# Kernel tuning notes

Measured on AMD Instinct MI355X. Metric: run time of the kernel, lower is better.

## Reference

```python
import jax, jax.numpy as jnp
import numpy as np

B, N, T, D = 4, 256, 64, 128
DR, DH = 32, 128  # d_relation, d_hidden


def setup_inputs() -> dict:
    key = jax.random.key(0)
    ks = jax.random.split(key, 12)
    s = 0.05
    return {
        "H": jax.random.normal(ks[0], (B, N, T, D), jnp.float32),
        "R": jax.random.normal(ks[1], (B, N, N, DR), jnp.float32),
        "delta_H": jax.random.normal(ks[2], (B, N, T, D), jnp.float32),
        # params (torch Linear convention: W @ x + b with W shape (out, in))
        "Wq": jax.random.normal(ks[3], (DH, D), jnp.float32) * s,
        "bq": jnp.zeros((DH,), jnp.float32),
        "Wk": jax.random.normal(ks[4], (DH, D), jnp.float32) * s,
        "bk": jnp.zeros((DH,), jnp.float32),
        "Wr": jax.random.normal(ks[5], (DH, DR), jnp.float32) * s,
        "br": jnp.zeros((DH,), jnp.float32),
        "Wf": jax.random.normal(ks[6], (D, 3 * D + DR), jnp.float32) * s,
        "bf": jnp.zeros((D,), jnp.float32),
        "gamma": jnp.ones((D,), jnp.float32),
        "beta": jnp.zeros((D,), jnp.float32),
    }


def reference(H, R, delta_H, Wq, bq, Wk, bk, Wr, br, Wf, bf, gamma, beta):
    Bm, Nn, Tt, Dd = H.shape
    dr = R.shape[-1]

    # projections (eval mode: dropout is identity)
    q = jnp.einsum('bitd,hd->bith', H, Wq) + bq           # (B,N,T,DH)
    k = jnp.einsum('bjtd,hd->bjth', H, Wk) + bk           # (B,N,T,DH)
    rproj = jnp.einsum('bijr,hr->bijh', R, Wr) + br       # (B,N,N,DH)

    # attn_score[b,i,j,t] = <q_i[t], k_j[t] + Wr(r_ij)> / sqrt(d_model)
    scores = (jnp.einsum('bith,bjth->bijt', q, k)
              + jnp.einsum('bith,bijh->bijt', q, rproj)) / jnp.sqrt(jnp.asarray(Dd, H.dtype))
    w = jax.nn.softmax(scores, axis=-1)                   # softmax over time t
    # exclude the j == i pair (original loop skips it)
    w = w * (1.0 - jnp.eye(Nn, dtype=w.dtype))[None, :, :, None]

    # fuse Linear decomposed over the concat [h_i, h_j, r_ij, sum_t delta_h_j]
    W1 = Wf[:, :Dd]                 # acts on h_i
    W2 = Wf[:, Dd:2 * Dd]           # acts on h_j
    W3 = Wf[:, 2 * Dd:2 * Dd + dr]  # acts on r_ij
    W4 = Wf[:, 2 * Dd + dr:]        # acts on delta sum

    A = jnp.einsum('bitd,ed->bite', H, W1)                       # (B,N,T,D)
    Bj = jnp.einsum('bjtd,ed->bjte', H, W2)                      # (B,N,T,D)
    Cij = jnp.einsum('bijr,er->bije', R, W3)                     # (B,N,N,D)
    Ej = jnp.einsum('bjd,ed->bje', delta_H.sum(axis=2), W4)      # (B,N,D)

    wsum = w.sum(axis=2)                                         # (B,N,T)
    z = ((A + bf) * wsum[..., None]
         + jnp.einsum('bijt,bjte->bite', w, Bj)
         + jnp.einsum('bijt,bije->bite', w, Cij)
         + jnp.einsum('bijt,bje->bite', w, Ej))

    # residual + LayerNorm over last dim
    x = H + z
    mu = x.mean(axis=-1, keepdims=True)
    var = x.var(axis=-1, keepdims=True)
    return (x - mu) / jnp.sqrt(var + 1e-5) * gamma + beta
```

## Files before the change

kernel.cpp:

```cpp
#include <hip/hip_runtime.h>

typedef __attribute__((ext_vector_type(4))) float f32x4;
typedef __attribute__((ext_vector_type(8))) short short8;

constexpr int NB = 4, NS = 256, NT = 64, ND = 128, NR = 32;
constexpr int WFR = 3 * ND + NR;
constexpr float SCALE = 0.08838834764831845f;

__device__ __forceinline__ unsigned short f2bf(float f) {
  unsigned x = __float_as_uint(f);
  return (unsigned short)((x + 0x7FFFu + ((x >> 16) & 1u)) >> 16);
}
__device__ __forceinline__ float bf2f(unsigned short u) {
  return __uint_as_float((unsigned)u << 16);
}

__global__ __launch_bounds__(256) void kP(const float* __restrict__ Wq,
    const float* __restrict__ Wk, const float* __restrict__ Wr,
    const float* __restrict__ br, const float* __restrict__ bq,
    const float* __restrict__ Wf,
    unsigned short* __restrict__ Wqb, unsigned short* __restrict__ Wkb,
    unsigned short* __restrict__ W1b, unsigned short* __restrict__ W2b,
    unsigned short* __restrict__ W3b, unsigned short* __restrict__ Wqrt,
    float* __restrict__ Gbias) {
  const int blk = blockIdx.x, tid = threadIdx.x;
  if (blk < 64) {
    const int which = blk >> 4;
    const int idx = ((blk & 15) * 256 + tid) * 4;
    const int e = idx >> 7, d = idx & 127;
    float4 v;
    unsigned short* dst;
    if (which == 0)      { v = *(const float4*)&Wq[idx];            dst = Wqb; }
    else if (which == 1) { v = *(const float4*)&Wk[idx];            dst = Wkb; }
    else if (which == 2) { v = *(const float4*)&Wf[e * WFR + d];        dst = W1b; }
    else                 { v = *(const float4*)&Wf[e * WFR + ND + d];   dst = W2b; }
    dst[idx + 0] = f2bf(v.x); dst[idx + 1] = f2bf(v.y);
    dst[idx + 2] = f2bf(v.z); dst[idx + 3] = f2bf(v.w);
  } else if (blk < 68) {
    const int idx = ((blk - 64) * 256 + tid) * 4;
    const int e = idx >> 5, r = idx & 31;
    float4 v = *(const float4*)&Wf[e * WFR + 2 * ND + r];
    W3b[idx + 0] = f2bf(v.x); W3b[idx + 1] = f2bf(v.y);
    W3b[idx + 2] = f2bf(v.z); W3b[idx + 3] = f2bf(v.w);
  } else {
    const int rr = blk - 68;
    __shared__ float Vl[128];
    __shared__ float gbl[128];
    if (tid < 128) {
      float v = 0.f;
      if (rr < 32) v = Wr[tid * 32 + rr];
      else if (rr == 32) v = br[tid];
      Vl[tid] = v;
      gbl[tid] = bq[tid] * v;
    }
    __syncthreads();
    if (tid < 128) {
      float acc = 0.f;
      #pragma unroll 8
      for (int h = 0; h < 128; ++h) acc += Wq[h * 128 + tid] * Vl[h];
      Wqrt[rr * 128 + tid] = f2bf(acc * SCALE);
    }
    if (tid == 0) {
      float g = 0.f;
      for (int h = 0; h < 128; ++h) g += gbl[h];
      Gbias[rr] = g * SCALE;
    }
  }
}

__global__ __launch_bounds__(128) void kA(const float* __restrict__ dH,
                                          const float* __restrict__ Wf,
                                          float* __restrict__ Ej) {
  __shared__ float ds[ND];
  const int bj = blockIdx.x;
  const int d = threadIdx.x;
  const float* p = dH + (size_t)bj * NT * ND + d;
  float s = 0.f;
  #pragma unroll 8
  for (int t = 0; t < NT; ++t) s += p[t * ND];
  ds[d] = s;
  __syncthreads();
  const float* w4 = Wf + (size_t)d * WFR + 2 * ND + NR;
  float acc = 0.f;
  #pragma unroll 8
  for (int dd = 0; dd < ND; ++dd) acc += ds[dd] * w4[dd];
  Ej[(size_t)bj * ND + d] = acc;
}

__global__ __launch_bounds__(256) void kR(const float* __restrict__ R,
                                          unsigned short* __restrict__ Rb,
                                          unsigned short* __restrict__ Rtb) {
  __shared__ unsigned short rt[256 * 34];
  const int bi = blockIdx.x, tid = threadIdx.x;
  const float* src = R + (size_t)bi * 8192;
  #pragma unroll
  for (int it = 0; it < 8; ++it) {
    const int idx = (tid + it * 256) * 4;
    const float4 v = *(const float4*)&src[idx];
    const unsigned short s0 = f2bf(v.x), s1 = f2bf(v.y);
    const unsigned short s2 = f2bf(v.z), s3 = f2bf(v.w);
    unsigned long long p = (unsigned long long)s0 | ((unsigned long long)s1 << 16)
                         | ((unsigned long long)s2 << 32) | ((unsigned long long)s3 << 48);
    *(unsigned long long*)&Rb[(size_t)bi * 8192 + idx] = p;
    const int j = idx >> 5, r = idx & 31;
    *(unsigned*)&rt[j * 34 + r]     = (unsigned)s0 | ((unsigned)s1 << 16);
    *(unsigned*)&rt[j * 34 + r + 2] = (unsigned)s2 | ((unsigned)s3 << 16);
  }
  __syncthreads();
  #pragma unroll
  for (int it = 0; it < 4; ++it) {
    const int flat = (tid + it * 256) * 8;
    const int r = flat >> 8, j0 = flat & 255;
    short8 o;
    #pragma unroll
    for (int u = 0; u < 8; ++u) o[u] = (short)rt[(j0 + u) * 34 + r];
    *(short8*)&Rtb[(size_t)bi * 8192 + flat] = o;
  }
}

__device__ __forceinline__ void gemm_tile(const short8 (&afr)[4][4],
    const unsigned short* __restrict__ Wp, int nt, int l15, int l4,
    f32x4 (&acc)[4]) {
  #pragma unroll
  for (int mt = 0; mt < 4; ++mt) acc[mt] = (f32x4){0.f, 0.f, 0.f, 0.f};
  #pragma unroll
  for (int kt = 0; kt < 4; ++kt) {
    short8 bfr = *(const short8*)(Wp + (16 * nt + l15) * 128 + 32 * kt + 8 * l4);
    #pragma unroll
    for (int mt = 0; mt < 4; ++mt)
      acc[mt] = __builtin_amdgcn_mfma_f32_16x16x32_bf16(afr[mt][kt], bfr, acc[mt], 0, 0, 0);
  }
}

__device__ __forceinline__ void gemm_tile2(const short8 (&afr)[2][4],
    const unsigned short* __restrict__ Wp, int nt, int l15, int l4,
    f32x4 (&acc)[2]) {
  #pragma unroll
  for (int mt = 0; mt < 2; ++mt) acc[mt] = (f32x4){0.f, 0.f, 0.f, 0.f};
  #pragma unroll
  for (int kt = 0; kt < 4; ++kt) {
    short8 bfr = *(const short8*)(Wp + (16 * nt + l15) * 128 + 32 * kt + 8 * l4);
    #pragma unroll
    for (int mt = 0; mt < 2; ++mt)
      acc[mt] = __builtin_amdgcn_mfma_f32_16x16x32_bf16(afr[mt][kt], bfr, acc[mt], 0, 0, 0);
  }
}

__global__ __launch_bounds__(256) void kB(const float* __restrict__ H,
    const unsigned short* __restrict__ W1b, const unsigned short* __restrict__ W2b,
    const unsigned short* __restrict__ Wqrt, const float* __restrict__ Gbias,
    const float* __restrict__ bf, const float* __restrict__ Ej,
    unsigned short* __restrict__ Apbb, unsigned short* __restrict__ BEb,
    unsigned short* __restrict__ Gb) {
  __shared__ unsigned short st[2][64 * 136];
  const int bn = blockIdx.x, tid = threadIdx.x;
  const int b = bn >> 8, n = bn & 255;
  const int lane = tid & 63, wv = tid >> 6;
  const int l15 = lane & 15, l4 = lane >> 4;
  short8 afr[4][4];
  const float* hb = H + (size_t)bn * (NT * ND);
  #pragma unroll
  for (int mt = 0; mt < 4; ++mt)
    #pragma unroll
    for (int kt = 0; kt < 4; ++kt) {
      const float* p = hb + (16 * mt + l15) * ND + 32 * kt + 8 * l4;
      float4 u0 = *(const float4*)p;
      float4 u1 = *(const float4*)(p + 4);
      short8 f;
      f[0] = (short)f2bf(u0.x); f[1] = (short)f2bf(u0.y);
      f[2] = (short)f2bf(u0.z); f[3] = (short)f2bf(u0.w);
      f[4] = (short)f2bf(u1.x); f[5] = (short)f2bf(u1.y);
      f[6] = (short)f2bf(u1.z); f[7] = (short)f2bf(u1.w);
      afr[mt][kt] = f;
    }
  f32x4 acc[4];
  #pragma unroll 1
  for (int pass = 0; pass < 2; ++pass) {
    const unsigned short* W = (pass == 0) ? W1b : W2b;
    unsigned short* buf = st[pass];
    #pragma unroll
    for (int n2 = 0; n2 < 2; ++n2) {
      const int nt = 2 * wv + n2, c = 16 * nt + l15;
      gemm_tile(afr, W, nt, l15, l4, acc);
      const float bias = (pass == 0) ? bf[c] : Ej[(size_t)bn * 128 + c];
      #pragma unroll
      for (int mt = 0; mt < 4; ++mt)
        #pragma unroll
        for (int jr = 0; jr < 4; ++jr)
          buf[(16 * mt + 4 * l4 + jr) * 136 + c] = f2bf(acc[mt][jr] + bias);
    }
  }
  if (wv < 3) {
    const int nt = wv, c = 16 * nt + l15;
    gemm_tile(afr, Wqrt, nt, l15, l4, acc);
    const float bias = Gbias[c];
    #pragma unroll
    for (int mt = 0; mt < 4; ++mt)
      #pragma unroll
      for (int jr = 0; jr < 4; ++jr) {
        const int tr = 16 * mt + 4 * l4 + jr;
        Gb[(size_t)bn * 3072 + tr * 48 + c] = f2bf(acc[mt][jr] + bias);
      }
  }
  __syncthreads();
  #pragma unroll
  for (int it = 0; it < 4; ++it) {
    const int flat = tid * 8 + it * 2048;
    const int row = flat >> 7, col = flat & 127;
    *(short8*)&Apbb[(size_t)bn * 8192 + flat] = *(const short8*)&st[0][row * 136 + col];
    *(short8*)&BEb[((size_t)(b * 64 + row) * 256 + n) * 128 + col] =
        *(const short8*)&st[1][row * 136 + col];
  }
}

__global__ __launch_bounds__(512) void kQK(const float* __restrict__ H,
    const unsigned short* __restrict__ Wqb, const unsigned short* __restrict__ Wkb,
    const float* __restrict__ bq, const float* __restrict__ bk,
    unsigned short* __restrict__ Sb) {
  __shared__ unsigned short qs[256 * 136];
  __shared__ unsigned short ks[256 * 136];
  const int bt = blockIdx.x;
  const int b = bt >> 6, t = bt & 63;
  const int tid = threadIdx.x, lane = tid & 63, wv = tid >> 6;
  const int l15 = lane & 15, l4 = lane >> 4;
  short8 afr[2][4];
  #pragma unroll
  for (int mt = 0; mt < 2; ++mt)
    #pragma unroll
    for (int kt = 0; kt < 4; ++kt) {
      const int n = 32 * wv + 16 * mt + l15;
      const float* p = &H[(((size_t)(b * 256 + n)) * 64 + t) * 128 + 32 * kt + 8 * l4];
      float4 u0 = *(const float4*)p;
      float4 u1 = *(const float4*)(p + 4);
      short8 f;
      f[0] = (short)f2bf(u0.x); f[1] = (short)f2bf(u0.y);
      f[2] = (short)f2bf(u0.z); f[3] = (short)f2bf(u0.w);
      f[4] = (short)f2bf(u1.x); f[5] = (short)f2bf(u1.y);
      f[6] = (short)f2bf(u1.z); f[7] = (short)f2bf(u1.w);
      afr[mt][kt] = f;
    }
  f32x4 acc[2];
  #pragma unroll 1
  for (int pass = 0; pass < 2; ++pass) {
    const unsigned short* W = (pass == 0) ? Wqb : Wkb;
    const float* bp = (pass == 0) ? bq : bk;
    unsigned short* dst = (pass == 0) ? qs : ks;
    #pragma unroll
    for (int nt = 0; nt < 8; ++nt) {
      gemm_tile2(afr, W, nt, l15, l4, acc);
      const int c = 16 * nt + l15;
      const float bias = bp[c];
      #pragma unroll
      for (int mt = 0; mt < 2; ++mt)
        #pragma unroll
        for (int jr = 0; jr < 4; ++jr)
          dst[(32 * wv + 16 * mt + 4 * l4 + jr) * 136 + c] = f2bf(acc[mt][jr] + bias);
    }
  }
  __syncthreads();
  short8 qa[2][4];
  #pragma unroll
  for (int mt = 0; mt < 2; ++mt)
    #pragma unroll
    for (int kt = 0; kt < 4; ++kt)
      qa[mt][kt] = *(const short8*)&qs[(32 * wv + 16 * mt + l15) * 136 + 32 * kt + 8 * l4];
  unsigned short* buf = qs + wv * (32 * 136);
  #pragma unroll 1
  for (int jh = 0; jh < 2; ++jh) {
    f32x4 sacc[2][8];
    #pragma unroll
    for (int mi = 0; mi < 2; ++mi)
      #pragma unroll
      for (int ntj = 0; ntj < 8; ++ntj) sacc[mi][ntj] = (f32x4){0.f, 0.f, 0.f, 0.f};
    #pragma unroll
    for (int kt = 0; kt < 4; ++kt) {
      short8 bb[8];
      #pragma unroll
      for (int ntj = 0; ntj < 8; ++ntj)
        bb[ntj] = *(const short8*)&ks[(16 * (8 * jh + ntj) + l15) * 136 + 32 * kt + 8 * l4];
      #pragma unroll
      for (int mi = 0; mi < 2; ++mi)
        #pragma unroll
        for (int ntj = 0; ntj < 8; ++ntj)
          sacc[mi][ntj] = __builtin_amdgcn_mfma_f32_16x16x32_bf16(qa[mi][kt], bb[ntj], sacc[mi][ntj], 0, 0, 0);
    }
    #pragma unroll
    for (int mi = 0; mi < 2; ++mi)
      #pragma unroll
      for (int ntj = 0; ntj < 8; ++ntj)
        #pragma unroll
        for (int jr = 0; jr < 4; ++jr)
          buf[(16 * mi + 4 * l4 + jr) * 136 + 16 * ntj + l15] =
              f2bf(sacc[mi][ntj][jr] * SCALE);
    #pragma unroll
    for (int it = 0; it < 8; ++it) {
      const int flat = lane * 8 + it * 512;
      const int row = flat >> 7, col = flat & 127;
      *(short8*)&Sb[((size_t)bt * 256 + 32 * wv + row) * 256 + 128 * jh + col] =
          *(const short8*)&buf[row * 136 + col];
    }
  }
}

__global__ __launch_bounds__(256) void kSM(
    const unsigned short* __restrict__ Gb, const unsigned short* __restrict__ Rb,
    const unsigned short* __restrict__ Rtb, const unsigned short* __restrict__ Sb,
    const unsigned short* __restrict__ W3b, unsigned short* __restrict__ Apbb,
    unsigned short* __restrict__ Wbw) {
  __shared__ unsigned short wl[64 * 264];
  __shared__ unsigned short Ml[4][16 * 40];
  __shared__ float wred[4][64];
  __shared__ float wsl[64];
  const int bi = blockIdx.x, b = bi >> 8, i = bi & 255;
  const int tid = threadIdx.x, lane = tid & 63, wv = tid >> 6;
  const int l15 = lane & 15, l4 = lane >> 4;
  const f32x4 zz = (f32x4){0.f, 0.f, 0.f, 0.f};

  #pragma unroll
  for (int it = 0; it < 8; ++it) {
    const int flat = tid * 8 + it * 2048;
    const int t = flat >> 8, col = flat & 255;
    *(short8*)&wl[t * 264 + col] =
        *(const short8*)&Sb[(((size_t)b * 64 + t) * 256 + i) * 256 + col];
  }

  short8 ga[4];
  #pragma unroll
  for (int mt = 0; mt < 4; ++mt)
    ga[mt] = *(const short8*)(Gb + ((size_t)bi * 64 + 16 * mt + l15) * 48 + 8 * l4);
  f32x4 acc[4][4];
  #pragma unroll
  for (int nt = 0; nt < 4; ++nt) {
    const int j = 64 * wv + 16 * nt + l15;
    short8 rb = *(const short8*)(Rb + ((size_t)bi * 256 + j) * 32 + 8 * l4);
    #pragma unroll
    for (int mt = 0; mt < 4; ++mt)
      acc[mt][nt] = __builtin_amdgcn_mfma_f32_16x16x32_bf16(ga[mt], rb, zz, 0, 0, 0);
  }
  float qbr[4][4];
  #pragma unroll
  for (int mt = 0; mt < 4; ++mt)
    #pragma unroll
    for (int jr = 0; jr < 4; ++jr)
      qbr[mt][jr] = bf2f(Gb[((size_t)bi * 64 + 16 * mt + 4 * l4 + jr) * 48 + 32]);

  __syncthreads();

  #pragma unroll
  for (int mt = 0; mt < 4; ++mt)
    #pragma unroll
    for (int nt = 0; nt < 4; ++nt)
      #pragma unroll
      for (int jr = 0; jr < 4; ++jr)
        acc[mt][nt][jr] += bf2f(wl[(16 * mt + 4 * l4 + jr) * 264 + 64 * wv + 16 * nt + l15])
                         + qbr[mt][jr];

  #pragma unroll
  for (int nt = 0; nt < 4; ++nt) {
    float mx = -1e30f;
    #pragma unroll
    for (int mt = 0; mt < 4; ++mt)
      #pragma unroll
      for (int jr = 0; jr < 4; ++jr) mx = fmaxf(mx, acc[mt][nt][jr]);
    mx = fmaxf(mx, __shfl_xor(mx, 16));
    mx = fmaxf(mx, __shfl_xor(mx, 32));
    float sm = 0.f;
    #pragma unroll
    for (int mt = 0; mt < 4; ++mt)
      #pragma unroll
      for (int jr = 0; jr < 4; ++jr) {
        const float e = __expf(acc[mt][nt][jr] - mx);
        acc[mt][nt][jr] = e;
        sm += e;
      }
    sm += __shfl_xor(sm, 16);
    sm += __shfl_xor(sm, 32);
    const int j = 64 * wv + 16 * nt + l15;
    const float inv = (j == i) ? 0.f : 1.f / sm;
    #pragma unroll
    for (int mt = 0; mt < 4; ++mt)
      #pragma unroll
      for (int jr = 0; jr < 4; ++jr) acc[mt][nt][jr] *= inv;
  }

  float part[4][4];
  #pragma unroll
  for (int mt = 0; mt < 4; ++mt)
    #pragma unroll
    for (int jr = 0; jr < 4; ++jr) {
      float s = 0.f;
      #pragma unroll
      for (int nt = 0; nt < 4; ++nt) s += acc[mt][nt][jr];
      part[mt][jr] = s;
    }
  #pragma unroll
  for (int m = 1; m < 16; m <<= 1)
    #pragma unroll
    for (int mt = 0; mt < 4; ++mt)
      #pragma unroll
      for (int jr = 0; jr < 4; ++jr) part[mt][jr] += __shfl_xor(part[mt][jr], m);
  if (l15 == 0) {
    #pragma unroll
    for (int mt = 0; mt < 4; ++mt)
      #pragma unroll
      for (int jr = 0; jr < 4; ++jr) wred[wv][16 * mt + 4 * l4 + jr] = part[mt][jr];
  }

  #pragma unroll
  for (int mt = 0; mt < 4; ++mt)
    #pragma unroll
    for (int nt = 0; nt < 4; ++nt)
      #pragma unroll
      for (int jr = 0; jr < 4; ++jr)
        wl[(16 * mt + 4 * l4 + jr) * 264 + 64 * wv + 16 * nt + l15] =
            f2bf(acc[mt][nt][jr]);

  __syncthreads();

  if (tid < 64) wsl[tid] = wred[0][tid] + wred[1][tid] + wred[2][tid] + wred[3][tid];

  #pragma unroll
  for (int it = 0; it < 8; ++it) {
    const int flat = tid * 8 + it * 2048;
    const int t = flat >> 8, j = flat & 255;
    *(short8*)&Wbw[(((size_t)(b * 64 + t)) * 256 + i) * 256 + j] =
        *(const short8*)&wl[t * 264 + j];
  }

  f32x4 mac[2];
  mac[0] = zz; mac[1] = zz;
  #pragma unroll
  for (int kt = 0; kt < 8; ++kt) {
    short8 a = *(const short8*)&wl[(16 * wv + l15) * 264 + 32 * kt + 8 * l4];
    #pragma unroll
    for (int nt = 0; nt < 2; ++nt) {
      short8 bb = *(const short8*)(Rtb + ((size_t)bi * 32 + 16 * nt + l15) * 256 + 32 * kt + 8 * l4);
      mac[nt] = __builtin_amdgcn_mfma_f32_16x16x32_bf16(a, bb, mac[nt], 0, 0, 0);
    }
  }
  #pragma unroll
  for (int nt = 0; nt < 2; ++nt)
    #pragma unroll
    for (int jr = 0; jr < 4; ++jr)
      Ml[wv][(4 * l4 + jr) * 40 + 16 * nt + l15] = f2bf(mac[nt][jr]);
  asm volatile("s_waitcnt lgkmcnt(0)" ::: "memory");
  short8 a2 = *(const short8*)&Ml[wv][l15 * 40 + 8 * l4];
  f32x4 tac[8];
  #pragma unroll
  for (int nt = 0; nt < 8; ++nt) {
    short8 w3 = *(const short8*)(W3b + (16 * nt + l15) * 32 + 8 * l4);
    tac[nt] = __builtin_amdgcn_mfma_f32_16x16x32_bf16(a2, w3, zz, 0, 0, 0);
  }
  __syncthreads();

  const size_t abase = (size_t)bi * 8192;
  #pragma unroll
  for (int it = 0; it < 4; ++it) {
    const int flat = tid * 8 + it * 2048;
    const int row = flat >> 7, col = flat & 127;
    *(short8*)&wl[row * 136 + col] = *(const short8*)&Apbb[abase + flat];
  }
  __syncthreads();
  #pragma unroll
  for (int jr = 0; jr < 4; ++jr) {
    const int t = 16 * wv + 4 * l4 + jr;
    const float ws = wsl[t];
    #pragma unroll
    for (int nt = 0; nt < 8; ++nt) {
      const int e = 16 * nt + l15;
      const int off = t * 136 + e;
      wl[off] = f2bf(bf2f(wl[off]) * ws + tac[nt][jr]);
    }
  }
  __syncthreads();
  #pragma unroll
  for (int it = 0; it < 4; ++it) {
    const int flat = tid * 8 + it * 2048;
    const int row = flat >> 7, col = flat & 127;
    *(short8*)&Apbb[abase + flat] = *(const short8*)&wl[row * 136 + col];
  }
}

__global__ __launch_bounds__(512) void kD(const unsigned short* __restrict__ Wb,
    const unsigned short* __restrict__ BEb, const unsigned short* __restrict__ zacc,
    const float* __restrict__ H, const float* __restrict__ gamma,
    const float* __restrict__ beta, float* __restrict__ out) {
  __shared__ unsigned short Bl[128 * 264];
  const int bt = blockIdx.x;
  const int b = bt >> 6, t = bt & 63;
  const int tid = threadIdx.x, lane = tid & 63, wv = tid >> 6;
  const int l15 = lane & 15, l4 = lane >> 4;
  {
    const int j = tid >> 1, eh = (tid & 1) * 64;
    const unsigned short* src = BEb + (size_t)bt * (256 * 128) + j * 128 + eh;
    #pragma unroll
    for (int eg = 0; eg < 8; ++eg) {
      short8 v = *(const short8*)(src + 8 * eg);
      #pragma unroll
      for (int u = 0; u < 8; ++u)
        Bl[(eh + 8 * eg + u) * 264 + j] = (unsigned short)v[u];
    }
  }
  __syncthreads();
  f32x4 acc[2][8];
  #pragma unroll
  for (int m2 = 0; m2 < 2; ++m2)
    #pragma unroll
    for (int nt = 0; nt < 8; ++nt) acc[m2][nt] = (f32x4){0.f, 0.f, 0.f, 0.f};
  #pragma unroll
  for (int kt = 0; kt < 8; ++kt) {
    short8 a[2];
    #pragma unroll
    for (int m2 = 0; m2 < 2; ++m2) {
      const int i = 32 * wv + 16 * m2 + l15;
      a[m2] = *(const short8*)(Wb + ((size_t)(b * 64 + t) * 256 + i) * 256 + 32 * kt + 8 * l4);
    }
    #pragma unroll
    for (int nt = 0; nt < 8; ++nt) {
      short8 bb = *(const short8*)(&Bl[(16 * nt + l15) * 264 + 32 * kt + 8 * l4]);
      #pragma unroll
      for (int m2 = 0; m2 < 2; ++m2)
        acc[m2][nt] = __builtin_amdgcn_mfma_f32_16x16x32_bf16(a[m2], bb, acc[m2][nt], 0, 0, 0);
    }
  }
  float gam[8], bet[8];
  #pragma unroll
  for (int nt = 0; nt < 8; ++nt) {
    const int e = 16 * nt + l15;
    gam[nt] = gamma[e];
    bet[nt] = beta[e];
  }
  #pragma unroll
  for (int m2 = 0; m2 < 2; ++m2)
    #pragma unroll
    for (int jr = 0; jr < 4; ++jr) {
      const int i = 32 * wv + 16 * m2 + 4 * l4 + jr;
      const size_t base = ((size_t)(b * 256 + i) * 64 + t) * 128;
      float x[8];
      float sm = 0.f, sq = 0.f;
      #pragma unroll
      for (int nt = 0; nt < 8; ++nt) {
        const int e = 16 * nt + l15;
        const float v = acc[m2][nt][jr] + bf2f(zacc[base + e]) + H[base + e];
        x[nt] = v;
        sm += v;
        sq += v * v;
      }
      #pragma unroll
      for (int m = 1; m < 16; m <<= 1) {
        sm += __shfl_xor(sm, m);
        sq += __shfl_xor(sq, m);
      }
      const float mu = sm * (1.f / 128.f);
      const float inv = rsqrtf(sq * (1.f / 128.f) - mu * mu + 1e-5f);
      #pragma unroll
      for (int nt = 0; nt < 8; ++nt)
        out[base + 16 * nt + l15] = (x[nt] - mu) * inv * gam[nt] + bet[nt];
    }
}

extern "C" void kernel_launch(void* const* d_in, const int* in_sizes, int n_in,
                              void* d_out, int out_size, void* d_ws, size_t ws_size,
                              hipStream_t stream) {
  (void)in_sizes; (void)n_in; (void)out_size; (void)ws_size;
  const float* H     = (const float*)d_in[0];
  const float* R     = (const float*)d_in[1];
  const float* dH    = (const float*)d_in[2];
  const float* Wq    = (const float*)d_in[3];
  const float* bq    = (const float*)d_in[4];
  const float* Wk    = (const float*)d_in[5];
  const float* bk    = (const float*)d_in[6];
  const float* Wr    = (const float*)d_in[7];
  const float* br    = (const float*)d_in[8];
  const float* Wf    = (const float*)d_in[9];
  const float* bf    = (const float*)d_in[10];
  const float* gamma = (const float*)d_in[11];
  const float* beta  = (const float*)d_in[12];
  float* out = (float*)d_out;
  char* w = (char*)d_ws;

  unsigned short* Wbw  = (unsigned short*)(w + 0);
  unsigned short* Sb   = (unsigned short*)(w + 33554432);
  unsigned short* Apbb = (unsigned short*)(w + 67108864);
  unsigned short* BEb  = (unsigned short*)(w + 83886080);
  unsigned short* Gb   = (unsigned short*)(w + 100663296);
  unsigned short* Rb   = (unsigned short*)(w + 106954752);
  unsigned short* Rtb  = (unsigned short*)(w + 123731968);
  float*          Ejb  = (float*)(w + 140509184);
  unsigned short* Wqb  = (unsigned short*)(w + 141033472);
  unsigned short* Wkb  = (unsigned short*)(w + 141066240);
  unsigned short* W1b  = (unsigned short*)(w + 141099008);
  unsigned short* W2b  = (unsigned short*)(w + 141131776);
  unsigned short* W3b  = (unsigned short*)(w + 141164544);
  unsigned short* Wqrt = (unsigned short*)(w + 141172736);
  float*          Gbs  = (float*)(w + 141185024);

  kP<<<dim3(116), dim3(256), 0, stream>>>(Wq, Wk, Wr, br, bq, Wf,
                                          Wqb, Wkb, W1b, W2b, W3b, Wqrt, Gbs);
  kA<<<dim3(NB * NS), dim3(128), 0, stream>>>(dH, Wf, Ejb);
  kR<<<dim3(NB * NS), dim3(256), 0, stream>>>(R, Rb, Rtb);
  kB<<<dim3(NB * NS), dim3(256), 0, stream>>>(H, W1b, W2b, Wqrt, Gbs,
                                              bf, Ejb, Apbb, BEb, Gb);
  kQK<<<dim3(NB * NT), dim3(512), 0, stream>>>(H, Wqb, Wkb, bq, bk, Sb);
  kSM<<<dim3(NB * NS), dim3(256), 0, stream>>>(Gb, Rb, Rtb, Sb, W3b, Apbb, Wbw);
  kD<<<dim3(NB * NT), dim3(512), 0, stream>>>(Wbw, BEb, Apbb, H, gamma, beta, out);
}
```

Measured before the change: 164.3 us.

## Fuse kB projections into kSM and kD, fold Ej term into weighted GEMM

Removes the standalone kB kernel. Its H@W1 (A term) and H@Wqrt (G term) projections are now computed inside kSM, with G staged in shared memory. The H@W2 (B term) projection is computed inside kD directly into its LDS tile. The Ej contribution is no longer added as a bias on B. Instead kA writes Ej transposed in bf16 and kSM multiplies it by the attention weights with extra MFMAs. This avoids writing and re-reading the large Apbb, BEb and Gb intermediates and saves one launch, in exchange for redundant H loads and extra MFMA work in kSM and kD.

```diff
diff --git a/kernel.cpp b/kernel.cpp
--- a/kernel.cpp
+++ b/kernel.cpp
@@ -70,9 +70,10 @@
 
 __global__ __launch_bounds__(128) void kA(const float* __restrict__ dH,
                                           const float* __restrict__ Wf,
-                                          float* __restrict__ Ej) {
+                                          unsigned short* __restrict__ Ejt) {
   __shared__ float ds[ND];
   const int bj = blockIdx.x;
+  const int b = bj >> 8, j = bj & 255;
   const int d = threadIdx.x;
   const float* p = dH + (size_t)bj * NT * ND + d;
   float s = 0.f;
@@ -84,7 +85,7 @@
   float acc = 0.f;
   #pragma unroll 8
   for (int dd = 0; dd < ND; ++dd) acc += ds[dd] * w4[dd];
-  Ej[(size_t)bj * ND + d] = acc;
+  Ejt[((size_t)b * 128 + d) * 256 + j] = f2bf(acc);
 }
 
 __global__ __launch_bounds__(256) void kR(const float* __restrict__ R,
@@ -146,73 +147,6 @@
   }
 }
 
-__global__ __launch_bounds__(256) void kB(const float* __restrict__ H,
-    const unsigned short* __restrict__ W1b, const unsigned short* __restrict__ W2b,
-    const unsigned short* __restrict__ Wqrt, const float* __restrict__ Gbias,
-    const float* __restrict__ bf, const float* __restrict__ Ej,
-    unsigned short* __restrict__ Apbb, unsigned short* __restrict__ BEb,
-    unsigned short* __restrict__ Gb) {
-  __shared__ unsigned short st[2][64 * 136];
-  const int bn = blockIdx.x, tid = threadIdx.x;
-  const int b = bn >> 8, n = bn & 255;
-  const int lane = tid & 63, wv = tid >> 6;
-  const int l15 = lane & 15, l4 = lane >> 4;
-  short8 afr[4][4];
-  const float* hb = H + (size_t)bn * (NT * ND);
-  #pragma unroll
-  for (int mt = 0; mt < 4; ++mt)
-    #pragma unroll
-    for (int kt = 0; kt < 4; ++kt) {
-      const float* p = hb + (16 * mt + l15) * ND + 32 * kt + 8 * l4;
-      float4 u0 = *(const float4*)p;
-      float4 u1 = *(const float4*)(p + 4);
-      short8 f;
-      f[0] = (short)f2bf(u0.x); f[1] = (short)f2bf(u0.y);
-      f[2] = (short)f2bf(u0.z); f[3] = (short)f2bf(u0.w);
-      f[4] = (short)f2bf(u1.x); f[5] = (short)f2bf(u1.y);
-      f[6] = (short)f2bf(u1.z); f[7] = (short)f2bf(u1.w);
-      afr[mt][kt] = f;
-    }
-  f32x4 acc[4];
-  #pragma unroll 1
-  for (int pass = 0; pass < 2; ++pass) {
-    const unsigned short* W = (pass == 0) ? W1b : W2b;
-    unsigned short* buf = st[pass];
-    #pragma unroll
-    for (int n2 = 0; n2 < 2; ++n2) {
-      const int nt = 2 * wv + n2, c = 16 * nt + l15;
-      gemm_tile(afr, W, nt, l15, l4, acc);
-      const float bias = (pass == 0) ? bf[c] : Ej[(size_t)bn * 128 + c];
-      #pragma unroll
-      for (int mt = 0; mt < 4; ++mt)
-        #pragma unroll
-        for (int jr = 0; jr < 4; ++jr)
-          buf[(16 * mt + 4 * l4 + jr) * 136 + c] = f2bf(acc[mt][jr] + bias);
-    }
-  }
-  if (wv < 3) {
-    const int nt = wv, c = 16 * nt + l15;
-    gemm_tile(afr, Wqrt, nt, l15, l4, acc);
-    const float bias = Gbias[c];
-    #pragma unroll
-    for (int mt = 0; mt < 4; ++mt)
-      #pragma unroll
-      for (int jr = 0; jr < 4; ++jr) {
-        const int tr = 16 * mt + 4 * l4 + jr;
-        Gb[(size_t)bn * 3072 + tr * 48 + c] = f2bf(acc[mt][jr] + bias);
-      }
-  }
-  __syncthreads();
-  #pragma unroll
-  for (int it = 0; it < 4; ++it) {
-    const int flat = tid * 8 + it * 2048;
-    const int row = flat >> 7, col = flat & 127;
-    *(short8*)&Apbb[(size_t)bn * 8192 + flat] = *(const short8*)&st[0][row * 136 + col];
-    *(short8*)&BEb[((size_t)(b * 64 + row) * 256 + n) * 128 + col] =
-        *(const short8*)&st[1][row * 136 + col];
-  }
-}
-
 __global__ __launch_bounds__(512) void kQK(const float* __restrict__ H,
     const unsigned short* __restrict__ Wqb, const unsigned short* __restrict__ Wkb,
     const float* __restrict__ bq, const float* __restrict__ bk,
@@ -303,11 +237,14 @@
 }
 
 __global__ __launch_bounds__(256) void kSM(
-    const unsigned short* __restrict__ Gb, const unsigned short* __restrict__ Rb,
+    const float* __restrict__ H, const unsigned short* __restrict__ Wqrt,
+    const float* __restrict__ Gbs, const unsigned short* __restrict__ W1b,
+    const float* __restrict__ bf, const unsigned short* __restrict__ Rb,
     const unsigned short* __restrict__ Rtb, const unsigned short* __restrict__ Sb,
-    const unsigned short* __restrict__ W3b, unsigned short* __restrict__ Apbb,
-    unsigned short* __restrict__ Wbw) {
+    const unsigned short* __restrict__ W3b, const unsigned short* __restrict__ Ejt,
+    unsigned short* __restrict__ Zb, unsigned short* __restrict__ Wbw) {
   __shared__ unsigned short wl[64 * 264];
+  __shared__ unsigned short Gl[64 * 56];
   __shared__ unsigned short Ml[4][16 * 40];
   __shared__ float wred[4][64];
   __shared__ float wsl[64];
@@ -324,10 +261,55 @@
         *(const short8*)&Sb[(((size_t)b * 64 + t) * 256 + i) * 256 + col];
   }
 
+  short8 hfr[4][4];
+  {
+    const float* hb = H + (size_t)bi * 8192;
+    #pragma unroll
+    for (int mt = 0; mt < 4; ++mt)
+      #pragma unroll
+      for (int kt = 0; kt < 4; ++kt) {
+        const float* p = hb + (16 * mt + l15) * ND + 32 * kt + 8 * l4;
+        float4 u0 = *(const float4*)p;
+        float4 u1 = *(const float4*)(p + 4);
+        short8 f;
+        f[0] = (short)f2bf(u0.x); f[1] = (short)f2bf(u0.y);
+        f[2] = (short)f2bf(u0.z); f[3] = (short)f2bf(u0.w);
+        f[4] = (short)f2bf(u1.x); f[5] = (short)f2bf(u1.y);
+        f[6] = (short)f2bf(u1.z); f[7] = (short)f2bf(u1.w);
+        hfr[mt][kt] = f;
+      }
+  }
+
+  f32x4 apacc[8];
+  #pragma unroll
+  for (int nt = 0; nt < 8; ++nt) {
+    apacc[nt] = zz;
+    #pragma unroll
+    for (int kt = 0; kt < 4; ++kt) {
+      short8 w1 = *(const short8*)(W1b + (16 * nt + l15) * 128 + 32 * kt + 8 * l4);
+      apacc[nt] = __builtin_amdgcn_mfma_f32_16x16x32_bf16(hfr[wv][kt], w1, apacc[nt], 0, 0, 0);
+    }
+  }
+  float bfv[8];
+  #pragma unroll
+  for (int nt = 0; nt < 8; ++nt) bfv[nt] = bf[16 * nt + l15];
+
+  if (wv < 3) {
+    f32x4 g[4];
+    gemm_tile(hfr, Wqrt, wv, l15, l4, g);
+    const float gb = Gbs[16 * wv + l15];
+    #pragma unroll
+    for (int mt = 0; mt < 4; ++mt)
+      #pragma unroll
+      for (int jr = 0; jr < 4; ++jr)
+        Gl[(16 * mt + 4 * l4 + jr) * 56 + 16 * wv + l15] = f2bf(g[mt][jr] + gb);
+  }
+  __syncthreads();
+
   short8 ga[4];
   #pragma unroll
   for (int mt = 0; mt < 4; ++mt)
-    ga[mt] = *(const short8*)(Gb + ((size_t)bi * 64 + 16 * mt + l15) * 48 + 8 * l4);
+    ga[mt] = *(const short8*)&Gl[(16 * mt + l15) * 56 + 8 * l4];
   f32x4 acc[4][4];
   #pragma unroll
   for (int nt = 0; nt < 4; ++nt) {
@@ -342,9 +324,7 @@
   for (int mt = 0; mt < 4; ++mt)
     #pragma unroll
     for (int jr = 0; jr < 4; ++jr)
-      qbr[mt][jr] = bf2f(Gb[((size_t)bi * 64 + 16 * mt + 4 * l4 + jr) * 48 + 32]);
-
-  __syncthreads();
+      qbr[mt][jr] = bf2f(Gl[(16 * mt + 4 * l4 + jr) * 56 + 32]);
 
   #pragma unroll
   for (int mt = 0; mt < 4; ++mt)
@@ -429,6 +409,9 @@
 
   f32x4 mac[2];
   mac[0] = zz; mac[1] = zz;
+  f32x4 m2[8];
+  #pragma unroll
+  for (int nt = 0; nt < 8; ++nt) m2[nt] = zz;
   #pragma unroll
   for (int kt = 0; kt < 8; ++kt) {
     short8 a = *(const short8*)&wl[(16 * wv + l15) * 264 + 32 * kt + 8 * l4];
@@ -436,6 +419,11 @@
     for (int nt = 0; nt < 2; ++nt) {
       short8 bb = *(const short8*)(Rtb + ((size_t)bi * 32 + 16 * nt + l15) * 256 + 32 * kt + 8 * l4);
       mac[nt] = __builtin_amdgcn_mfma_f32_16x16x32_bf16(a, bb, mac[nt], 0, 0, 0);
+    }
+    #pragma unroll
+    for (int nt = 0; nt < 8; ++nt) {
+      short8 eb = *(const short8*)(Ejt + ((size_t)b * 128 + 16 * nt + l15) * 256 + 32 * kt + 8 * l4);
+      m2[nt] = __builtin_amdgcn_mfma_f32_16x16x32_bf16(a, eb, m2[nt], 0, 0, 0);
     }
   }
   #pragma unroll
@@ -453,53 +441,67 @@
   }
   __syncthreads();
 
-  const size_t abase = (size_t)bi * 8192;
+  #pragma unroll
+  for (int jr = 0; jr < 4; ++jr) {
+    const int t = 16 * wv + 4 * l4 + jr;
+    const float ws = wsl[t];
+    #pragma unroll
+    for (int nt = 0; nt < 8; ++nt) {
+      const int e = 16 * nt + l15;
+      wl[t * 136 + e] = f2bf((apacc[nt][jr] + bfv[nt]) * ws + tac[nt][jr] + m2[nt][jr]);
+    }
+  }
+  __syncthreads();
   #pragma unroll
   for (int it = 0; it < 4; ++it) {
     const int flat = tid * 8 + it * 2048;
     const int row = flat >> 7, col = flat & 127;
-    *(short8*)&wl[row * 136 + col] = *(const short8*)&Apbb[abase + flat];
-  }
-  __syncthreads();
-  #pragma unroll
-  for (int jr = 0; jr < 4; ++jr) {
-    const int t = 16 * wv + 4 * l4 + jr;
-    const float ws = wsl[t];
-    #pragma unroll
-    for (int nt = 0; nt < 8; ++nt) {
-      const int e = 16 * nt + l15;
-      const int off = t * 136 + e;
-      wl[off] = f2bf(bf2f(wl[off]) * ws + tac[nt][jr]);
-    }
-  }
-  __syncthreads();
-  #pragma unroll
-  for (int it = 0; it < 4; ++it) {
-    const int flat = tid * 8 + it * 2048;
-    const int row = flat >> 7, col = flat & 127;
-    *(short8*)&Apbb[abase + flat] = *(const short8*)&wl[row * 136 + col];
+    *(short8*)&Zb[(size_t)bi * 8192 + flat] = *(const short8*)&wl[row * 136 + col];
   }
 }
 
 __global__ __launch_bounds__(512) void kD(const unsigned short* __restrict__ Wb,
-    const unsigned short* __restrict__ BEb, const unsigned short* __restrict__ zacc,
-    const float* __restrict__ H, const float* __restrict__ gamma,
+    const float* __restrict__ H, const unsigned short* __restrict__ W2b,
+    const unsigned short* __restrict__ zacc, const float* __restrict__ gamma,
     const float* __restrict__ beta, float* __restrict__ out) {
   __shared__ unsigned short Bl[128 * 264];
   const int bt = blockIdx.x;
   const int b = bt >> 6, t = bt & 63;
   const int tid = threadIdx.x, lane = tid & 63, wv = tid >> 6;
   const int l15 = lane & 15, l4 = lane >> 4;
-  {
-    const int j = tid >> 1, eh = (tid & 1) * 64;
-    const unsigned short* src = BEb + (size_t)bt * (256 * 128) + j * 128 + eh;
-    #pragma unroll
-    for (int eg = 0; eg < 8; ++eg) {
-      short8 v = *(const short8*)(src + 8 * eg);
-      #pragma unroll
-      for (int u = 0; u < 8; ++u)
-        Bl[(eh + 8 * eg + u) * 264 + j] = (unsigned short)v[u];
-    }
+  short8 hfr[2][4];
+  #pragma unroll
+  for (int mt = 0; mt < 2; ++mt)
+    #pragma unroll
+    for (int kt = 0; kt < 4; ++kt) {
+      const int j = 32 * wv + 16 * mt + l15;
+      const float* p = &H[(((size_t)(b * 256 + j)) * 64 + t) * 128 + 32 * kt + 8 * l4];
+      float4 u0 = *(const float4*)p;
+      float4 u1 = *(const float4*)(p + 4);
+      short8 f;
+      f[0] = (short)f2bf(u0.x); f[1] = (short)f2bf(u0.y);
+      f[2] = (short)f2bf(u0.z); f[3] = (short)f2bf(u0.w);
+      f[4] = (short)f2bf(u1.x); f[5] = (short)f2bf(u1.y);
+      f[6] = (short)f2bf(u1.z); f[7] = (short)f2bf(u1.w);
+      hfr[mt][kt] = f;
+    }
+  #pragma unroll
+  for (int nt = 0; nt < 8; ++nt) {
+    f32x4 be[2];
+    be[0] = (f32x4){0.f, 0.f, 0.f, 0.f};
+    be[1] = (f32x4){0.f, 0.f, 0.f, 0.f};
+    #pragma unroll
+    for (int kt = 0; kt < 4; ++kt) {
+      short8 w2 = *(const short8*)(W2b + (16 * nt + l15) * 128 + 32 * kt + 8 * l4);
+      #pragma unroll
+      for (int mt = 0; mt < 2; ++mt)
+        be[mt] = __builtin_amdgcn_mfma_f32_16x16x32_bf16(hfr[mt][kt], w2, be[mt], 0, 0, 0);
+    }
+    #pragma unroll
+    for (int mt = 0; mt < 2; ++mt)
+      #pragma unroll
+      for (int jr = 0; jr < 4; ++jr)
+        Bl[(16 * nt + l15) * 264 + 32 * wv + 16 * mt + 4 * l4 + jr] = f2bf(be[mt][jr]);
   }
   __syncthreads();
   f32x4 acc[2][8];
@@ -581,27 +583,24 @@
 
   unsigned short* Wbw  = (unsigned short*)(w + 0);
   unsigned short* Sb   = (unsigned short*)(w + 33554432);
-  unsigned short* Apbb = (unsigned short*)(w + 67108864);
-  unsigned short* BEb  = (unsigned short*)(w + 83886080);
-  unsigned short* Gb   = (unsigned short*)(w + 100663296);
-  unsigned short* Rb   = (unsigned short*)(w + 106954752);
-  unsigned short* Rtb  = (unsigned short*)(w + 123731968);
-  float*          Ejb  = (float*)(w + 140509184);
-  unsigned short* Wqb  = (unsigned short*)(w + 141033472);
-  unsigned short* Wkb  = (unsigned short*)(w + 141066240);
-  unsigned short* W1b  = (unsigned short*)(w + 141099008);
-  unsigned short* W2b  = (unsigned short*)(w + 141131776);
-  unsigned short* W3b  = (unsigned short*)(w + 141164544);
-  unsigned short* Wqrt = (unsigned short*)(w + 141172736);
-  float*          Gbs  = (float*)(w + 141185024);
+  unsigned short* Zb   = (unsigned short*)(w + 67108864);
+  unsigned short* Rb   = (unsigned short*)(w + 83886080);
+  unsigned short* Rtb  = (unsigned short*)(w + 100663296);
+  unsigned short* Ejt  = (unsigned short*)(w + 117440512);
+  unsigned short* Wqb  = (unsigned short*)(w + 117702656);
+  unsigned short* Wkb  = (unsigned short*)(w + 117735424);
+  unsigned short* W1b  = (unsigned short*)(w + 117768192);
+  unsigned short* W2b  = (unsigned short*)(w + 117800960);
+  unsigned short* W3b  = (unsigned short*)(w + 117833728);
+  unsigned short* Wqrt = (unsigned short*)(w + 117841920);
+  float*          Gbs  = (float*)(w + 117854208);
 
   kP<<<dim3(116), dim3(256), 0, stream>>>(Wq, Wk, Wr, br, bq, Wf,
                                           Wqb, Wkb, W1b, W2b, W3b, Wqrt, Gbs);
-  kA<<<dim3(NB * NS), dim3(128), 0, stream>>>(dH, Wf, Ejb);
+  kA<<<dim3(NB * NS), dim3(128), 0, stream>>>(dH, Wf, Ejt);
   kR<<<dim3(NB * NS), dim3(256), 0, stream>>>(R, Rb, Rtb);
-  kB<<<dim3(NB * NS), dim3(256), 0, stream>>>(H, W1b, W2b, Wqrt, Gbs,
-                                              bf, Ejb, Apbb, BEb, Gb);
   kQK<<<dim3(NB * NT), dim3(512), 0, stream>>>(H, Wqb, Wkb, bq, bk, Sb);
-  kSM<<<dim3(NB * NS), dim3(256), 0, stream>>>(Gb, Rb, Rtb, Sb, W3b, Apbb, Wbw);
-  kD<<<dim3(NB * NT), dim3(512), 0, stream>>>(Wbw, BEb, Apbb, H, gamma, beta, out);
-}
+  kSM<<<dim3(NB * NS), dim3(256), 0, stream>>>(H, Wqrt, Gbs, W1b, bf, Rb, Rtb,
+                                               Sb, W3b, Ejt, Zb, Wbw);
+  kD<<<dim3(NB * NT), dim3(512), 0, stream>>>(Wbw, H, W2b, Zb, gamma, beta, out);
+}
```

Result: slower. 212.3 us (+29.2%).
